# Performance work log

Measured on AMD Instinct MI355X. Metric: run time of the kernel, lower is better.

The kernel has to match this reference:

```python
import jax, jax.numpy as jnp
import numpy as np

N_NODES = 20000
D_FEAT = 256
N_SUPPORT = 3
N_EDGES = 320000
OUT_DIM = 256


def setup_inputs() -> dict:
    key = jax.random.key(0)
    k1, k2, k3, k4, k5 = jax.random.split(key, 5)
    x = jax.random.normal(k1, (N_NODES, D_FEAT), dtype=jnp.float32)
    edge_src = jax.random.randint(k2, (N_SUPPORT, N_EDGES), 0, N_NODES, dtype=jnp.int64 if jax.config.jax_enable_x64 else jnp.int32).astype(jnp.int32)
    edge_dst = jax.random.randint(k3, (N_SUPPORT, N_EDGES), 0, N_NODES, dtype=jnp.int32)
    edge_w = jax.random.uniform(k4, (N_SUPPORT, N_EDGES), dtype=jnp.float32)
    # dense weight over concatenated supports: (support * input_dim, output_dim)
    W = jax.random.normal(k5, (N_SUPPORT * D_FEAT, OUT_DIM), dtype=jnp.float32) * (1.0 / np.sqrt(N_SUPPORT * D_FEAT))
    return {"x": x, "edge_src": edge_src, "edge_dst": edge_dst, "edge_w": edge_w, "W": W}


def reference(x, edge_src, edge_dst, edge_w, W):
    # supports_i = A_i @ x  (sparse adjacency as weighted edge list, per support)
    n = x.shape[0]
    supports = []
    for s in range(edge_src.shape[0]):  # small fixed number of relations
        msgs = x[edge_src[s]] * edge_w[s][:, None]              # [E, d]
        supports.append(jax.ops.segment_sum(msgs, edge_dst[s], num_segments=n))
    h = jnp.concatenate(supports, axis=1)                        # [N, support*d]
    # activation='linear' -> identity; bias=False
    return h @ W                                                 # [N, output_dim]
```

## Files before the change

### kernel.cpp

```cpp
#include <hip/hip_runtime.h>

#define N_NODES 20000
#define D_FEAT 256
#define N_SUPPORT 3
#define N_EDGES 320000
#define OUT_DIM 256
#define TOTAL_E (N_SUPPORT * N_EDGES)
#define CAP 64
#define KDIM (N_SUPPORT * D_FEAT)
#define NBUCKET (N_SUPPORT * N_NODES)
#define GM_ROWS 128
#define GM_BLOCKS ((N_NODES + GM_ROWS - 1) / GM_ROWS)

typedef __attribute__((ext_vector_type(8))) short short8;
typedef __attribute__((ext_vector_type(8))) unsigned short ushort8;
typedef __attribute__((ext_vector_type(4))) float f32x4;

__device__ inline unsigned short f2bf(float f) {
    unsigned int u = __float_as_uint(f);
    u += 0x7fff + ((u >> 16) & 1);
    return (unsigned short)(u >> 16);
}

#define NB_X (N_NODES / 4)
#define NB_W (N_SUPPORT * D_FEAT)
#define NB_F (TOTAL_E / 256)

__global__ void __launch_bounds__(256) prep1(const float* __restrict__ x, const float* __restrict__ W,
        unsigned int* __restrict__ xq, float* __restrict__ scl, unsigned short* __restrict__ wt) {
    const int bid = blockIdx.x;
    const int tid = threadIdx.x;
    if (bid < NB_X) {
        const int row = bid * 4 + (tid >> 6);
        const int lane = tid & 63;
        float4 v = ((const float4*)x)[row * 64 + lane];
        float m = fmaxf(fmaxf(fabsf(v.x), fabsf(v.y)), fmaxf(fabsf(v.z), fabsf(v.w)));
#pragma unroll
        for (int d = 1; d < 64; d <<= 1) m = fmaxf(m, __shfl_xor(m, d, 64));
        const float inv = (m > 0.f) ? 127.0f / m : 0.f;
        int q0 = (int)rintf(v.x * inv) + 128;
        int q1 = (int)rintf(v.y * inv) + 128;
        int q2 = (int)rintf(v.z * inv) + 128;
        int q3 = (int)rintf(v.w * inv) + 128;
        unsigned int pk = (unsigned int)q0 | ((unsigned int)q1 << 8)
                        | ((unsigned int)q2 << 16) | ((unsigned int)q3 << 24);
        xq[row * 64 + lane] = pk;
        if (lane == 0) scl[row] = m * (1.0f / 127.0f);
    } else {
        const int row = bid - NB_X;
        const int s = row >> 8, k = row & 255;
        wt[((size_t)s * OUT_DIM + tid) * D_FEAT + k] = f2bf(W[(size_t)row * OUT_DIM + tid]);
    }
}

__global__ void __launch_bounds__(256) prep2(const int* __restrict__ src, const int* __restrict__ dst,
        const float* __restrict__ w, const float* __restrict__ scl,
        int* __restrict__ cursor, unsigned int* __restrict__ epack) {
    const int i = blockIdx.x * 256 + threadIdx.x;
    if (i >= TOTAL_E) return;
    const int s = i / N_EDGES;
    const int sv = src[i];
    const int b = s * N_NODES + dst[i];
    const int pos = atomicAdd(&cursor[b], 1);
    if (pos < CAP) {
        const float wq = w[i] * scl[sv];
        epack[(size_t)b * CAP + pos] = (unsigned int)sv | (((unsigned int)f2bf(wq)) << 16);
    }
}

__global__ void __launch_bounds__(256) aggregate(
        const unsigned char* __restrict__ xq, const int* __restrict__ cursor,
        const unsigned int* __restrict__ epack, unsigned short* __restrict__ hb) {
    const int b = blockIdx.x * 8 + (threadIdx.x >> 5);
    const int l32 = threadIdx.x & 31;
    const int xoff = l32 * 8;
    const int s = b / N_NODES;
    const int node = b - s * N_NODES;

    int cnt = cursor[b]; if (cnt > CAP) cnt = CAP;
    const unsigned int* ep = epack + (size_t)b * CAP;

    float a[8];
#pragma unroll
    for (int j = 0; j < 8; ++j) a[j] = 0.f;
    float sw = 0.f;

    int it = 0;
    for (; it + 3 < cnt; it += 4) {
        const uint4 pk = *(const uint4*)(ep + it);
        const uint2 u0 = *(const uint2*)(xq + ((size_t)(pk.x & 0xFFFFu) << 8) + xoff);
        const uint2 u1 = *(const uint2*)(xq + ((size_t)(pk.y & 0xFFFFu) << 8) + xoff);
        const uint2 u2 = *(const uint2*)(xq + ((size_t)(pk.z & 0xFFFFu) << 8) + xoff);
        const uint2 u3 = *(const uint2*)(xq + ((size_t)(pk.w & 0xFFFFu) << 8) + xoff);
        const float w0 = __uint_as_float(pk.x & 0xFFFF0000u);
        const float w1 = __uint_as_float(pk.y & 0xFFFF0000u);
        const float w2 = __uint_as_float(pk.z & 0xFFFF0000u);
        const float w3 = __uint_as_float(pk.w & 0xFFFF0000u);
        sw += w0 + w1 + w2 + w3;
#pragma unroll
        for (int j = 0; j < 4; ++j) {
            const int sh = 8 * j;
            a[j]     += w0 * (float)((u0.x >> sh) & 0xffu) + w1 * (float)((u1.x >> sh) & 0xffu)
                      + w2 * (float)((u2.x >> sh) & 0xffu) + w3 * (float)((u3.x >> sh) & 0xffu);
            a[4 + j] += w0 * (float)((u0.y >> sh) & 0xffu) + w1 * (float)((u1.y >> sh) & 0xffu)
                      + w2 * (float)((u2.y >> sh) & 0xffu) + w3 * (float)((u3.y >> sh) & 0xffu);
        }
    }
    for (; it < cnt; ++it) {
        const unsigned int pe = ep[it];
        const uint2 u = *(const uint2*)(xq + ((size_t)(pe & 0xFFFFu) << 8) + xoff);
        const float wv = __uint_as_float(pe & 0xFFFF0000u);
        sw += wv;
#pragma unroll
        for (int j = 0; j < 4; ++j) {
            const int sh = 8 * j;
            a[j]     += wv * (float)((u.x >> sh) & 0xffu);
            a[4 + j] += wv * (float)((u.y >> sh) & 0xffu);
        }
    }

    ushort8 o;
    const float bias = 128.f * sw;
#pragma unroll
    for (int j = 0; j < 8; ++j) o[j] = f2bf(a[j] - bias);
    *(ushort8*)(hb + (size_t)node * KDIM + s * D_FEAT + xoff) = o;
}

__global__ void __launch_bounds__(512) gemm_h(
        const unsigned short* __restrict__ hb, const unsigned short* __restrict__ wt,
        float* __restrict__ out) {
    __shared__ unsigned short bs[OUT_DIM][136];
    const int n0 = blockIdx.x * GM_ROWS;
    const int wid = threadIdx.x >> 6;
    const int lane = threadIdx.x & 63;
    const int cit = lane & 15;
    const int kgrp = (lane >> 4) * 8;
    const bool valid = (n0 + wid * 16) < N_NODES;
    const int arow_idx = valid ? (n0 + wid * 16 + cit) : 0;
    const short* arow = (const short*)hb + (size_t)arow_idx * KDIM + kgrp;

    f32x4 acc[16];
#pragma unroll
    for (int j = 0; j < 16; ++j) acc[j] = (f32x4){0.f, 0.f, 0.f, 0.f};

    for (int kc = 0; kc < 6; ++kc) {
        const int s = kc >> 1;
        const int kb = (kc & 1) * 128;
        if (kc) __syncthreads();
        for (int i = threadIdx.x; i < 4096; i += 512) {
            const int n = i >> 4;
            const int k8 = (i & 15) << 3;
            *(ushort8*)&bs[n][k8] =
                *(const ushort8*)(wt + ((size_t)s * OUT_DIM + n) * D_FEAT + kb + k8);
        }
        __syncthreads();

#pragma unroll
        for (int ks = 0; ks < 4; ++ks) {
            short8 av = *(const short8*)(arow + kc * 128 + ks * 32);
#pragma unroll
            for (int nt = 0; nt < 16; ++nt) {
                short8 bv = *(const short8*)&bs[nt * 16 + cit][ks * 32 + kgrp];
                acc[nt] = __builtin_amdgcn_mfma_f32_16x16x32_bf16(av, bv, acc[nt], 0, 0, 0);
            }
        }
    }

    if (valid) {
        const int rbase = (lane >> 4) * 4;
#pragma unroll
        for (int nt = 0; nt < 16; ++nt) {
            const int col = nt * 16 + cit;
#pragma unroll
            for (int r = 0; r < 4; ++r) {
                out[(size_t)(n0 + wid * 16 + rbase + r) * OUT_DIM + col] = acc[nt][r];
            }
        }
    }
}

extern "C" void kernel_launch(void* const* d_in, const int* in_sizes, int n_in,
                              void* d_out, int out_size, void* d_ws, size_t ws_size,
                              hipStream_t stream) {
    const float* x        = (const float*)d_in[0];
    const int*   edge_src = (const int*)d_in[1];
    const int*   edge_dst = (const int*)d_in[2];
    const float* edge_w   = (const float*)d_in[3];
    const float* W        = (const float*)d_in[4];
    float* out = (float*)d_out;

    char* ws = (char*)d_ws;
    unsigned int*   xq     = (unsigned int*)(ws);
    float*          scl    = (float*)(ws + 5120000);
    unsigned short* wt     = (unsigned short*)(ws + 5200000);
    int*            cursor = (int*)(ws + 5593216);
    unsigned int*   epack  = (unsigned int*)(ws + 5833216);
    unsigned short* hb     = (unsigned short*)(ws + 21193216);

    hipMemsetAsync(cursor, 0, 240000, stream);

    prep1<<<NB_X + NB_W, 256, 0, stream>>>(x, W, xq, scl, wt);
    prep2<<<NB_F, 256, 0, stream>>>(edge_src, edge_dst, edge_w, scl, cursor, epack);

    aggregate<<<NBUCKET / 8, 256, 0, stream>>>((const unsigned char*)xq, cursor, epack, hb);

    gemm_h<<<GM_BLOCKS, 512, 0, stream>>>(hb, wt, out);
}
```

Measured before the change: 132.4 us.

## Replace global-atomic edge bucketing with two-pass binned shared-memory sort

Edge bucketing by destination is split into two passes. First, blocks group edges into 250 destination bins through shared-memory staging and batched global appends. Second, one block per bin scatters the records into per-node slots using shared-memory counters. This replaces roughly a million scattered global atomics on the per-node cursor array, and makes that array's memset unnecessary. The cost is an extra kernel launch, an intermediate bin buffer, and a fixed bin capacity of 4608 that could drop edges if a bin overflows.

```diff
diff --git a/kernel.cpp b/kernel.cpp
--- a/kernel.cpp
+++ b/kernel.cpp
@@ -12,6 +12,13 @@
 #define GM_ROWS 128
 #define GM_BLOCKS ((N_NODES + GM_ROWS - 1) / GM_ROWS)
 
+#define NBIN 250
+#define BINW 80
+#define LCAP 30
+#define BINCAP 4608
+#define PA_BATCH 4096
+#define PA_BLOCKS ((TOTAL_E + PA_BATCH - 1) / PA_BATCH)
+
 typedef __attribute__((ext_vector_type(8))) short short8;
 typedef __attribute__((ext_vector_type(8))) unsigned short ushort8;
 typedef __attribute__((ext_vector_type(4))) float f32x4;
@@ -24,7 +31,6 @@
 
 #define NB_X (N_NODES / 4)
 #define NB_W (N_SUPPORT * D_FEAT)
-#define NB_F (TOTAL_E / 256)
 
 __global__ void __launch_bounds__(256) prep1(const float* __restrict__ x, const float* __restrict__ W,
         unsigned int* __restrict__ xq, float* __restrict__ scl, unsigned short* __restrict__ wt) {
@@ -53,18 +59,86 @@
     }
 }
 
-__global__ void __launch_bounds__(256) prep2(const int* __restrict__ src, const int* __restrict__ dst,
+__global__ void __launch_bounds__(256) passA(const int* __restrict__ src, const int* __restrict__ dst,
         const float* __restrict__ w, const float* __restrict__ scl,
-        int* __restrict__ cursor, unsigned int* __restrict__ epack) {
-    const int i = blockIdx.x * 256 + threadIdx.x;
-    if (i >= TOTAL_E) return;
-    const int s = i / N_EDGES;
-    const int sv = src[i];
-    const int b = s * N_NODES + dst[i];
-    const int pos = atomicAdd(&cursor[b], 1);
-    if (pos < CAP) {
-        const float wq = w[i] * scl[sv];
-        epack[(size_t)b * CAP + pos] = (unsigned int)sv | (((unsigned int)f2bf(wq)) << 16);
+        int* __restrict__ gtail, uint2* __restrict__ gbin) {
+    __shared__ int lcnt[NBIN];
+    __shared__ uint2 lbuf[NBIN][LCAP];
+    const int tid = threadIdx.x;
+
+    for (int i = tid; i < NBIN; i += 256) lcnt[i] = 0;
+    __syncthreads();
+
+    const int e0 = blockIdx.x * PA_BATCH;
+#pragma unroll
+    for (int k = 0; k < PA_BATCH / 256; ++k) {
+        const int e = e0 + k * 256 + tid;
+        if (e < TOTAL_E) {
+            const int s = e / N_EDGES;
+            const int sv = src[e];
+            const int dv = dst[e];
+            const float wq = w[e] * scl[sv];
+            const int bin = dv / BINW;
+            uint2 rec;
+            rec.x = (unsigned int)sv | (((unsigned int)f2bf(wq)) << 16);
+            rec.y = (unsigned int)(s * BINW + (dv - bin * BINW));
+            const int pos = atomicAdd(&lcnt[bin], 1);
+            if (pos < LCAP) {
+                lbuf[bin][pos] = rec;
+            } else {
+                const int g = atomicAdd(&gtail[bin], 1);
+                if (g < BINCAP) gbin[(size_t)bin * BINCAP + g] = rec;
+            }
+        }
+    }
+    __syncthreads();
+
+    const int wid = tid >> 6;
+    const int lane = tid & 63;
+    for (int bin = wid; bin < NBIN; bin += 4) {
+        int n = lcnt[bin]; if (n > LCAP) n = LCAP;
+        int base = 0;
+        if (lane == 0 && n > 0) base = atomicAdd(&gtail[bin], n);
+        base = __shfl(base, 0, 64);
+        if (lane < n) {
+            const int g = base + lane;
+            if (g < BINCAP) gbin[(size_t)bin * BINCAP + g] = lbuf[bin][lane];
+        }
+    }
+}
+
+__global__ void __launch_bounds__(256) passB(const int* __restrict__ gtail,
+        const uint2* __restrict__ gbin, int* __restrict__ cursor,
+        unsigned int* __restrict__ epack) {
+    __shared__ int lcnt2[N_SUPPORT * BINW];
+    const int bin = blockIdx.x;
+    const int tid = threadIdx.x;
+
+    for (int i = tid; i < N_SUPPORT * BINW; i += 256) lcnt2[i] = 0;
+    __syncthreads();
+
+    int m = gtail[bin]; if (m > BINCAP) m = BINCAP;
+    const uint2* gb = gbin + (size_t)bin * BINCAP;
+
+    for (int i = tid; i < m; i += 256) {
+        const uint2 r = gb[i];
+        const int lb = (int)r.y;
+        const int pos = atomicAdd(&lcnt2[lb], 1);
+        if (pos < CAP) {
+            const int s = lb / BINW;
+            const int dl = lb - s * BINW;
+            const int g = s * N_NODES + bin * BINW + dl;
+            epack[(size_t)g * CAP + pos] = r.x;
+        }
+    }
+    __syncthreads();
+
+    for (int lb = tid; lb < N_SUPPORT * BINW; lb += 256) {
+        const int s = lb / BINW;
+        const int dl = lb - s * BINW;
+        const int g = s * N_NODES + bin * BINW + dl;
+        int c = lcnt2[lb]; if (c > CAP) c = CAP;
+        cursor[g] = c;
     }
 }
 
@@ -195,12 +269,15 @@
     unsigned short* wt     = (unsigned short*)(ws + 5200000);
     int*            cursor = (int*)(ws + 5593216);
     unsigned int*   epack  = (unsigned int*)(ws + 5833216);
-    unsigned short* hb     = (unsigned short*)(ws + 21193216);
-
-    hipMemsetAsync(cursor, 0, 240000, stream);
+    int*            gtail  = (int*)(ws + 21193216);
+    uint2*          gbin   = (uint2*)(ws + 21194240);
+    unsigned short* hb     = (unsigned short*)(ws + 30410240);
+
+    hipMemsetAsync(gtail, 0, 1024, stream);
 
     prep1<<<NB_X + NB_W, 256, 0, stream>>>(x, W, xq, scl, wt);
-    prep2<<<NB_F, 256, 0, stream>>>(edge_src, edge_dst, edge_w, scl, cursor, epack);
+    passA<<<PA_BLOCKS, 256, 0, stream>>>(edge_src, edge_dst, edge_w, scl, gtail, gbin);
+    passB<<<NBIN, 256, 0, stream>>>(gtail, gbin, cursor, epack);
 
     aggregate<<<NBUCKET / 8, 256, 0, stream>>>((const unsigned char*)xq, cursor, epack, hb);
 
```

Measured after the change: 316.3 us. 2.39x slower.

## Bucket edges into per-window sub-lists then compact to cut atomic contention

Applied to the files above, without the earlier changes.

Edge binning now uses NWIN=8 separate cursor/list sets chosen by block index, so atomics from different block windows hit different counters. A new compact kernel merges the eight small lists per bucket into one CAP-sized list for the aggregate kernel. prep1 also processes four rows per wave to raise work per block. This adds a kernel launch, an eightfold larger memset, and extra list traffic. Each window list holds at most 16 entries, so edges beyond that are silently dropped, and ep1 aliases hb in the workspace.

```diff
diff --git a/kernel.cpp b/kernel.cpp
--- a/kernel.cpp
+++ b/kernel.cpp
@@ -7,6 +7,8 @@
 #define OUT_DIM 256
 #define TOTAL_E (N_SUPPORT * N_EDGES)
 #define CAP 64
+#define CAPX 16
+#define NWIN 8
 #define KDIM (N_SUPPORT * D_FEAT)
 #define NBUCKET (N_SUPPORT * N_NODES)
 #define GM_ROWS 128
@@ -22,7 +24,7 @@
     return (unsigned short)(u >> 16);
 }
 
-#define NB_X (N_NODES / 4)
+#define NB_X (N_NODES / 16)
 #define NB_W (N_SUPPORT * D_FEAT)
 #define NB_F (TOTAL_E / 256)
 
@@ -31,21 +33,33 @@
     const int bid = blockIdx.x;
     const int tid = threadIdx.x;
     if (bid < NB_X) {
-        const int row = bid * 4 + (tid >> 6);
+        const int wid = tid >> 6;
         const int lane = tid & 63;
-        float4 v = ((const float4*)x)[row * 64 + lane];
-        float m = fmaxf(fmaxf(fabsf(v.x), fabsf(v.y)), fmaxf(fabsf(v.z), fabsf(v.w)));
-#pragma unroll
-        for (int d = 1; d < 64; d <<= 1) m = fmaxf(m, __shfl_xor(m, d, 64));
-        const float inv = (m > 0.f) ? 127.0f / m : 0.f;
-        int q0 = (int)rintf(v.x * inv) + 128;
-        int q1 = (int)rintf(v.y * inv) + 128;
-        int q2 = (int)rintf(v.z * inv) + 128;
-        int q3 = (int)rintf(v.w * inv) + 128;
-        unsigned int pk = (unsigned int)q0 | ((unsigned int)q1 << 8)
-                        | ((unsigned int)q2 << 16) | ((unsigned int)q3 << 24);
-        xq[row * 64 + lane] = pk;
-        if (lane == 0) scl[row] = m * (1.0f / 127.0f);
+        const int row0 = bid * 16 + wid * 4;
+        float4 v[4];
+        float m[4];
+#pragma unroll
+        for (int r = 0; r < 4; ++r) {
+            v[r] = ((const float4*)x)[(size_t)(row0 + r) * 64 + lane];
+            m[r] = fmaxf(fmaxf(fabsf(v[r].x), fabsf(v[r].y)), fmaxf(fabsf(v[r].z), fabsf(v[r].w)));
+        }
+#pragma unroll
+        for (int d = 1; d < 64; d <<= 1) {
+#pragma unroll
+            for (int r = 0; r < 4; ++r) m[r] = fmaxf(m[r], __shfl_xor(m[r], d, 64));
+        }
+#pragma unroll
+        for (int r = 0; r < 4; ++r) {
+            const float inv = (m[r] > 0.f) ? 127.0f / m[r] : 0.f;
+            int q0 = (int)rintf(v[r].x * inv) + 128;
+            int q1 = (int)rintf(v[r].y * inv) + 128;
+            int q2 = (int)rintf(v[r].z * inv) + 128;
+            int q3 = (int)rintf(v[r].w * inv) + 128;
+            unsigned int pk = (unsigned int)q0 | ((unsigned int)q1 << 8)
+                            | ((unsigned int)q2 << 16) | ((unsigned int)q3 << 24);
+            xq[(size_t)(row0 + r) * 64 + lane] = pk;
+            if (lane == 0) scl[row0 + r] = m[r] * (1.0f / 127.0f);
+        }
     } else {
         const int row = bid - NB_X;
         const int s = row >> 8, k = row & 255;
@@ -53,23 +67,57 @@
     }
 }
 
-__global__ void __launch_bounds__(256) prep2(const int* __restrict__ src, const int* __restrict__ dst,
-        const float* __restrict__ w, const float* __restrict__ scl,
-        int* __restrict__ cursor, unsigned int* __restrict__ epack) {
+__global__ void __launch_bounds__(256) fill_win(const int* __restrict__ src,
+        const int* __restrict__ dst, const float* __restrict__ w, const float* __restrict__ scl,
+        int* __restrict__ cur8, unsigned int* __restrict__ ep1) {
     const int i = blockIdx.x * 256 + threadIdx.x;
     if (i >= TOTAL_E) return;
+    const int win = blockIdx.x & (NWIN - 1);
     const int s = i / N_EDGES;
     const int sv = src[i];
     const int b = s * N_NODES + dst[i];
-    const int pos = atomicAdd(&cursor[b], 1);
-    if (pos < CAP) {
+    const int pos = atomicAdd(&cur8[win * NBUCKET + b], 1);
+    if (pos < CAPX) {
         const float wq = w[i] * scl[sv];
-        epack[(size_t)b * CAP + pos] = (unsigned int)sv | (((unsigned int)f2bf(wq)) << 16);
-    }
+        ep1[((size_t)win * NBUCKET + b) * CAPX + pos] =
+            (unsigned int)sv | (((unsigned int)f2bf(wq)) << 16);
+    }
+}
+
+__global__ void __launch_bounds__(256) compact(const int* __restrict__ cur8,
+        const unsigned int* __restrict__ ep1, int* __restrict__ cnt2,
+        unsigned int* __restrict__ ep2) {
+    const int b = blockIdx.x * 8 + (threadIdx.x >> 5);
+    const int l32 = threadIdx.x & 31;
+
+    int myc = 0;
+    if (l32 < NWIN) {
+        int c = cur8[l32 * NBUCKET + b];
+        myc = (c > CAPX) ? CAPX : c;
+    }
+    int cx[NWIN], off[NWIN];
+    int tot = 0;
+#pragma unroll
+    for (int xw = 0; xw < NWIN; ++xw) {
+        cx[xw] = __shfl(myc, xw, 32);
+        off[xw] = tot;
+        tot += cx[xw];
+    }
+    if (tot > CAP) tot = CAP;
+
+    for (int i = l32; i < tot; i += 32) {
+        int xw = 0, idx = 0;
+#pragma unroll
+        for (int t = 0; t < NWIN; ++t) {
+            if (i >= off[t] && i < off[t] + cx[t]) { xw = t; idx = i - off[t]; }
+        }
+        ep2[(size_t)b * CAP + i] = ep1[((size_t)xw * NBUCKET + b) * CAPX + idx];
+    }
+    if (l32 == 0) cnt2[b] = tot;
 }
 
 __global__ void __launch_bounds__(256) aggregate(
-        const unsigned char* __restrict__ xq, const int* __restrict__ cursor,
+        const unsigned char* __restrict__ xq, const int* __restrict__ cnt2,
         const unsigned int* __restrict__ epack, unsigned short* __restrict__ hb) {
     const int b = blockIdx.x * 8 + (threadIdx.x >> 5);
     const int l32 = threadIdx.x & 31;
@@ -77,7 +125,7 @@
     const int s = b / N_NODES;
     const int node = b - s * N_NODES;
 
-    int cnt = cursor[b]; if (cnt > CAP) cnt = CAP;
+    int c = cnt2[b]; if (c > CAP) c = CAP;
     const unsigned int* ep = epack + (size_t)b * CAP;
 
     float a[8];
@@ -86,7 +134,7 @@
     float sw = 0.f;
 
     int it = 0;
-    for (; it + 3 < cnt; it += 4) {
+    for (; it + 3 < c; it += 4) {
         const uint4 pk = *(const uint4*)(ep + it);
         const uint2 u0 = *(const uint2*)(xq + ((size_t)(pk.x & 0xFFFFu) << 8) + xoff);
         const uint2 u1 = *(const uint2*)(xq + ((size_t)(pk.y & 0xFFFFu) << 8) + xoff);
@@ -106,7 +154,7 @@
                       + w2 * (float)((u2.y >> sh) & 0xffu) + w3 * (float)((u3.y >> sh) & 0xffu);
         }
     }
-    for (; it < cnt; ++it) {
+    for (; it < c; ++it) {
         const unsigned int pe = ep[it];
         const uint2 u = *(const uint2*)(xq + ((size_t)(pe & 0xFFFFu) << 8) + xoff);
         const float wv = __uint_as_float(pe & 0xFFFF0000u);
@@ -190,19 +238,22 @@
     float* out = (float*)d_out;
 
     char* ws = (char*)d_ws;
-    unsigned int*   xq     = (unsigned int*)(ws);
-    float*          scl    = (float*)(ws + 5120000);
-    unsigned short* wt     = (unsigned short*)(ws + 5200000);
-    int*            cursor = (int*)(ws + 5593216);
-    unsigned int*   epack  = (unsigned int*)(ws + 5833216);
-    unsigned short* hb     = (unsigned short*)(ws + 21193216);
-
-    hipMemsetAsync(cursor, 0, 240000, stream);
+    unsigned int*   xq    = (unsigned int*)(ws);
+    float*          scl   = (float*)(ws + 5120000);
+    unsigned short* wt    = (unsigned short*)(ws + 5200000);
+    int*            cur8  = (int*)(ws + 5593216);
+    int*            cnt2  = (int*)(ws + 7513216);
+    unsigned int*   ep2   = (unsigned int*)(ws + 7753216);
+    unsigned int*   ep1   = (unsigned int*)(ws + 23113216);
+    unsigned short* hb    = (unsigned short*)(ws + 23113216);
+
+    hipMemsetAsync(cur8, 0, 1920000, stream);
 
     prep1<<<NB_X + NB_W, 256, 0, stream>>>(x, W, xq, scl, wt);
-    prep2<<<NB_F, 256, 0, stream>>>(edge_src, edge_dst, edge_w, scl, cursor, epack);
-
-    aggregate<<<NBUCKET / 8, 256, 0, stream>>>((const unsigned char*)xq, cursor, epack, hb);
+    fill_win<<<NB_F, 256, 0, stream>>>(edge_src, edge_dst, edge_w, scl, cur8, ep1);
+    compact<<<NBUCKET / 8, 256, 0, stream>>>(cur8, ep1, cnt2, ep2);
+
+    aggregate<<<NBUCKET / 8, 256, 0, stream>>>((const unsigned char*)xq, cnt2, ep2, hb);
 
     gemm_h<<<GM_BLOCKS, 512, 0, stream>>>(hb, wt, out);
 }
```

Measured after the change: 129.7 us, median of 2. 2.1% less time.
